# Optimization experiments

Hardware: AMD Instinct MI355X
Metric: run time of the kernel (lower is better)

The kernel has to match this reference:

```python
import jax, jax.numpy as jnp
import numpy as np
import math

B, S, H, N = 64, 512, 768, 16
C_COMP, C_REL = 5, 3
P = N * (N - 1)
LN_EPS = 1e-5

# ordered pair indices (i, j), i != j, row-major like the torch double loop
_PAIR_I, _PAIR_J = np.nonzero(~np.eye(N, dtype=bool))
_PAIR_I = jnp.asarray(_PAIR_I)
_PAIR_J = jnp.asarray(_PAIR_J)


def setup_inputs() -> dict:
    key = jax.random.key(0)
    ks = jax.random.split(key, 20)
    sc = 0.02
    p = lambda k, shape: (jax.random.normal(k, shape, jnp.float32) * sc)
    return {
        "last_hidden_state": jax.random.normal(ks[0], (B, S, H), jnp.float32),
        "span_starts": jax.random.randint(ks[1], (B, N), 0, 480).astype(jnp.int32),
        "span_lengths": jax.random.randint(ks[2], (B, N), 0, 31).astype(jnp.int32),
        "components": jax.random.randint(ks[3], (B, N), 0, C_COMP).astype(jnp.int32),
        "relations": jax.random.randint(ks[4], (B, P), 0, C_REL).astype(jnp.int32),
        # comp_classifier: Linear(H,512) -> Tanh -> Linear(512,C_COMP)
        "comp_w1": p(ks[5], (H, 512)), "comp_b1": jnp.zeros((512,), jnp.float32),
        "comp_w2": p(ks[6], (512, C_COMP)), "comp_b2": jnp.zeros((C_COMP,), jnp.float32),
        # Attention(H, H), no bias
        "wq": p(ks[7], (H, H)), "wk": p(ks[8], (H, H)), "wv": p(ks[9], (H, H)),
        # LayerNorm(H)
        "ln_g": jnp.ones((H,), jnp.float32), "ln_b": jnp.zeros((H,), jnp.float32),
        # rel_classifier: Linear(2H,512) -> Tanh -> Linear(512,C_REL)
        "rel_w1": p(ks[10], (2 * H, 512)), "rel_b1": jnp.zeros((512,), jnp.float32),
        "rel_w2": p(ks[11], (512, C_REL)), "rel_b2": jnp.zeros((C_REL,), jnp.float32),
    }


def _ce_mean(logits, gold):
    # logits [M, C], gold [M] -> scalar mean cross entropy
    logp = jax.nn.log_softmax(logits, axis=-1)
    return -jnp.mean(jnp.take_along_axis(logp, gold[:, None].astype(jnp.int32), axis=-1))


def reference(last_hidden_state, span_starts, span_lengths, components, relations,
              comp_w1, comp_b1, comp_w2, comp_b2,
              wq, wk, wv, ln_g, ln_b,
              rel_w1, rel_b1, rel_w2, rel_b2):
    # --- per-span mean pooling (inclusive end = start + length), masked+vectorized ---
    pos = jnp.arange(S)
    ends = span_starts + span_lengths
    mask = ((pos[None, None, :] >= span_starts[:, :, None]) &
            (pos[None, None, :] <= ends[:, :, None])).astype(jnp.float32)  # [B,N,S]
    lens = (span_lengths + 1).astype(jnp.float32)
    pooled = jnp.einsum('bns,bsh->bnh', mask, last_hidden_state) / lens[:, :, None]  # [B,N,H]
    # dropout(p=0.2) is identity in eval mode

    # --- component classifier ---
    comp_logits = jnp.tanh(pooled @ comp_w1 + comp_b1) @ comp_w2 + comp_b2  # [B,N,C_COMP]

    # --- small self-attention over spans ---
    q = pooled @ wq; k = pooled @ wk; v = pooled @ wv
    scores = jax.nn.softmax(jnp.einsum('bnd,bmd->bnm', q, k) / math.sqrt(H), axis=-1)
    attn = jnp.einsum('bnm,bmh->bnh', scores, v)

    # --- residual + layernorm ---
    x = pooled + attn
    mu = jnp.mean(x, axis=-1, keepdims=True)
    var = jnp.mean((x - mu) ** 2, axis=-1, keepdims=True)
    x = (x - mu) * jax.lax.rsqrt(var + LN_EPS) * ln_g + ln_b  # [B,N,H]

    # --- O(N^2) pairwise relation classification (ordered pairs i != j) ---
    pair_feat = jnp.concatenate([x[:, _PAIR_I, :], x[:, _PAIR_J, :]], axis=-1)  # [B,P,2H]
    rel_logits = jnp.tanh(pair_feat @ rel_w1 + rel_b1) @ rel_w2 + rel_b2  # [B,P,C_REL]

    loss_comp = _ce_mean(comp_logits.reshape(-1, C_COMP), components.reshape(-1))
    loss_rel = _ce_mean(rel_logits.reshape(-1, C_REL), relations.reshape(-1))
    return (comp_logits.reshape(-1, C_COMP), rel_logits.reshape(-1, C_REL), loss_comp, loss_rel)
```

## Files before the change

### kernel.cpp

```cpp
#include <hip/hip_runtime.h>

#define BB 64
#define SS 512
#define HH 768
#define NSPAN 16
#define PP 240
#define CCOMP 5
#define CREL 3

typedef unsigned short u16;
typedef __attribute__((ext_vector_type(8))) short bf16x8;
typedef __attribute__((ext_vector_type(4))) float f32x4;

__device__ __forceinline__ u16 f2bf(float f) {
    union { float f; unsigned int i; } v; v.f = f;
    unsigned int x = v.i;
    unsigned int lsb = (x >> 16) & 1u;
    x += 0x7fffu + lsb;
    return (u16)(x >> 16);
}

__global__ __launch_bounds__(256) void prep_kernel(
    const float* __restrict__ cw1, const float* __restrict__ wq,
    const float* __restrict__ wk, const float* __restrict__ wv,
    const float* __restrict__ rw1, u16* __restrict__ wcat_t, u16* __restrict__ relw_t) {
    int blk = blockIdx.x;
    const float* W; int ldw, nt; u16* outp;
    if (blk < 384)        {             W = cw1; ldw = 512; nt = 16; outp = wcat_t; }
    else if (blk < 960)   { blk -= 384; W = wq;  ldw = 768; nt = 24; outp = wcat_t + (size_t)512 * 768; }
    else if (blk < 1536)  { blk -= 960; W = wk;  ldw = 768; nt = 24; outp = wcat_t + (size_t)1280 * 768; }
    else if (blk < 2112)  { blk -= 1536; W = wv; ldw = 768; nt = 24; outp = wcat_t + (size_t)2048 * 768; }
    else if (blk < 2496)  { blk -= 2112; W = rw1; ldw = 512; nt = 16; outp = relw_t; }
    else                  { blk -= 2496; W = rw1 + (size_t)768 * 512; ldw = 512; nt = 16; outp = relw_t + (size_t)512 * 768; }
    int tk = blk / nt, tn = blk % nt;
    int k0 = tk * 32, n0 = tn * 32;
    __shared__ u16 Ls[32][36];
    int tid = threadIdx.x;
    int tx = tid & 31, ty = tid >> 5;
#pragma unroll
    for (int r = 0; r < 4; ++r) {
        int k = ty + r * 8;
        Ls[tx][k] = f2bf(W[(size_t)(k0 + k) * ldw + n0 + tx]);
    }
    __syncthreads();
#pragma unroll
    for (int r = 0; r < 4; ++r) {
        int n = ty + r * 8;
        outp[(size_t)(n0 + n) * 768 + k0 + tx] = Ls[n][tx];
    }
}

__global__ __launch_bounds__(256) void pool_kernel(
    const float* __restrict__ lhs, const int* __restrict__ starts,
    const int* __restrict__ lens, float* __restrict__ pooled, u16* __restrict__ pooled_bf) {
    int bn = blockIdx.x;
    int b = bn >> 4;
    int st = starts[bn];
    int ln = lens[bn];
    int tid = threadIdx.x;
    const float* base = lhs + ((size_t)b * SS + st) * HH;
    float a0 = 0.f, a1 = 0.f, a2 = 0.f;
    for (int s = 0; s <= ln; ++s) {
        const float* row = base + (size_t)s * HH;
        a0 += row[tid];
        a1 += row[tid + 256];
        a2 += row[tid + 512];
    }
    float inv = 1.0f / (float)(ln + 1);
    a0 *= inv; a1 *= inv; a2 *= inv;
    float* out = pooled + (size_t)bn * HH;
    u16* outb = pooled_bf + (size_t)bn * HH;
    out[tid] = a0;       out[tid + 256] = a1;       out[tid + 512] = a2;
    outb[tid] = f2bf(a0); outb[tid + 256] = f2bf(a1); outb[tid + 512] = f2bf(a2);
}

__device__ __forceinline__ void gemm_mfma_tile(
    const u16* __restrict__ A, const u16* __restrict__ Bt,
    float* __restrict__ C, int ldc, int row0, int ccol0,
    const float* __restrict__ bias, int act) {
    __shared__ u16 As[64][72];
    __shared__ u16 Bs[64][72];
    int tid = threadIdx.x;
    int lane = tid & 63, w = tid >> 6;
    int q = lane >> 4, l15 = lane & 15;
    int wm = (w & 1) * 32, wn = (w >> 1) * 32;
    int r = tid >> 2, c0 = (tid & 3) * 16;
    const u16* ga = A + (size_t)(row0 + r) * 768 + c0;
    const u16* gb = Bt + (size_t)(ccol0 + r) * 768 + c0;
    f32x4 acc[2][2];
#pragma unroll
    for (int i = 0; i < 2; ++i)
#pragma unroll
        for (int j = 0; j < 2; ++j) acc[i][j] = (f32x4){0.f, 0.f, 0.f, 0.f};

    for (int k0 = 0; k0 < 768; k0 += 64) {
        uint4 va0 = *(const uint4*)(ga + k0);
        uint4 va1 = *(const uint4*)(ga + k0 + 8);
        uint4 vb0 = *(const uint4*)(gb + k0);
        uint4 vb1 = *(const uint4*)(gb + k0 + 8);
        __syncthreads();
        *(uint4*)(&As[r][c0]) = va0;
        *(uint4*)(&As[r][c0 + 8]) = va1;
        *(uint4*)(&Bs[r][c0]) = vb0;
        *(uint4*)(&Bs[r][c0 + 8]) = vb1;
        __syncthreads();
#pragma unroll
        for (int ks = 0; ks < 2; ++ks) {
            bf16x8 a0 = *(const bf16x8*)(&As[wm + l15][ks * 32 + q * 8]);
            bf16x8 a1 = *(const bf16x8*)(&As[wm + 16 + l15][ks * 32 + q * 8]);
            bf16x8 b0 = *(const bf16x8*)(&Bs[wn + l15][ks * 32 + q * 8]);
            bf16x8 b1 = *(const bf16x8*)(&Bs[wn + 16 + l15][ks * 32 + q * 8]);
            acc[0][0] = __builtin_amdgcn_mfma_f32_16x16x32_bf16(a0, b0, acc[0][0], 0, 0, 0);
            acc[0][1] = __builtin_amdgcn_mfma_f32_16x16x32_bf16(a0, b1, acc[0][1], 0, 0, 0);
            acc[1][0] = __builtin_amdgcn_mfma_f32_16x16x32_bf16(a1, b0, acc[1][0], 0, 0, 0);
            acc[1][1] = __builtin_amdgcn_mfma_f32_16x16x32_bf16(a1, b1, acc[1][1], 0, 0, 0);
        }
    }
#pragma unroll
    for (int tm = 0; tm < 2; ++tm)
#pragma unroll
        for (int tn = 0; tn < 2; ++tn)
#pragma unroll
            for (int reg = 0; reg < 4; ++reg) {
                int rr = row0 + wm + tm * 16 + q * 4 + reg;
                int cc = ccol0 + wn + tn * 16 + l15;
                float v = acc[tm][tn][reg];
                if (bias) v += bias[cc];
                if (act) v = tanhf(v);
                C[(size_t)rr * ldc + cc] = v;
            }
}

__global__ __launch_bounds__(256) void gemm_pw_kernel(
    const u16* __restrict__ pooled_bf, const u16* __restrict__ wcat_t,
    const float* __restrict__ comp_b1, float* __restrict__ y2) {
    int ccol0 = blockIdx.x * 64;
    int row0 = blockIdx.y * 64;
    int act = (ccol0 < 512);
    gemm_mfma_tile(pooled_bf, wcat_t, y2, 2816, row0, ccol0, act ? comp_b1 : nullptr, act);
}

__global__ __launch_bounds__(256) void gemm_z_kernel(
    const u16* __restrict__ x_bf, const u16* __restrict__ relw_t, float* __restrict__ Z) {
    int ccol0 = blockIdx.x * 64;
    int row0 = blockIdx.y * 64;
    gemm_mfma_tile(x_bf, relw_t, Z, 1024, row0, ccol0, nullptr, 0);
}

__global__ __launch_bounds__(256) void attn_ln_kernel(
    const float* __restrict__ y2, const float* __restrict__ pooled,
    const float* __restrict__ ln_g, const float* __restrict__ ln_b,
    float* __restrict__ x, u16* __restrict__ x_bf) {
    __shared__ float ks[16][772];
    __shared__ float Ssm[16][17];
    int b = blockIdx.x;
    int tid = threadIdx.x;
    int n = tid >> 4;
    int hl = tid & 15;

    for (int u = 0; u < 48; ++u) {
        int h = hl + (u << 4);
        ks[n][h] = y2[((size_t)(b * 16 + n)) * 2816 + 1280 + h];
    }
    __syncthreads();

    int m = tid & 15;
    const float* qrow = y2 + ((size_t)(b * 16 + n)) * 2816 + 512;
    float dot = 0.f;
    for (int h = 0; h < 768; h += 4) {
        float4 qv = *(const float4*)(qrow + h);
        float4 kv = *(const float4*)(&ks[m][h]);
        dot += qv.x * kv.x + qv.y * kv.y + qv.z * kv.z + qv.w * kv.w;
    }
    float sval = dot * 0.03608439182435161f;
    float mx = sval;
#pragma unroll
    for (int off = 8; off >= 1; off >>= 1) mx = fmaxf(mx, __shfl_xor(mx, off, 16));
    float pexp = __expf(sval - mx);
    float psum = pexp;
#pragma unroll
    for (int off = 8; off >= 1; off >>= 1) psum += __shfl_xor(psum, off, 16);
    Ssm[n][m] = pexp / psum;
    __syncthreads();

    for (int u = 0; u < 48; ++u) {
        int h = hl + (u << 4);
        ks[n][h] = y2[((size_t)(b * 16 + n)) * 2816 + 2048 + h];
    }
    __syncthreads();

    float sc[16];
#pragma unroll
    for (int mm = 0; mm < 16; ++mm) sc[mm] = Ssm[n][mm];
    int row = b * 16 + n;
    const float* prow = pooled + (size_t)row * HH;
    float xv[48];
    float ssum = 0.f, ssq = 0.f;
    for (int u = 0; u < 48; ++u) {
        int h = hl + (u << 4);
        float a = 0.f;
#pragma unroll
        for (int mm = 0; mm < 16; ++mm) a += sc[mm] * ks[mm][h];
        float v = prow[h] + a;
        xv[u] = v;
        ssum += v;
        ssq += v * v;
    }
#pragma unroll
    for (int off = 8; off >= 1; off >>= 1) {
        ssum += __shfl_xor(ssum, off, 16);
        ssq += __shfl_xor(ssq, off, 16);
    }
    float mu = ssum * (1.0f / 768.0f);
    float var = ssq * (1.0f / 768.0f) - mu * mu;
    float rs = rsqrtf(var + 1e-5f);
    float* xrow = x + (size_t)row * HH;
    u16* xrow_bf = x_bf + (size_t)row * HH;
    for (int u = 0; u < 48; ++u) {
        int h = hl + (u << 4);
        float v = (xv[u] - mu) * rs * ln_g[h] + ln_b[h];
        xrow[h] = v;
        xrow_bf[h] = f2bf(v);
    }
}

__global__ __launch_bounds__(256) void comp_head_kernel(
    const float* __restrict__ y2, const float* __restrict__ w2,
    const float* __restrict__ b2, const int* __restrict__ gold,
    float* __restrict__ out, float* __restrict__ partial) {
    __shared__ float red[4];
    int wave = threadIdx.x >> 6, lane = threadIdx.x & 63;
    int row = blockIdx.x * 4 + wave;
    const float* hrow = y2 + (size_t)row * 2816;
    float acc[CCOMP] = {0.f, 0.f, 0.f, 0.f, 0.f};
#pragma unroll
    for (int t = 0; t < 8; ++t) {
        int c = lane + (t << 6);
        float h = hrow[c];
#pragma unroll
        for (int cc = 0; cc < CCOMP; ++cc) acc[cc] += h * w2[c * CCOMP + cc];
    }
#pragma unroll
    for (int cc = 0; cc < CCOMP; ++cc)
#pragma unroll
        for (int off = 32; off >= 1; off >>= 1) acc[cc] += __shfl_down(acc[cc], off);
    if (lane == 0) {
        float l[CCOMP];
        float mx = -1e30f;
#pragma unroll
        for (int cc = 0; cc < CCOMP; ++cc) { l[cc] = acc[cc] + b2[cc]; mx = fmaxf(mx, l[cc]); }
        float se = 0.f;
#pragma unroll
        for (int cc = 0; cc < CCOMP; ++cc) se += __expf(l[cc] - mx);
        float lse = __logf(se) + mx;
        red[wave] = lse - l[gold[row]];
#pragma unroll
        for (int cc = 0; cc < CCOMP; ++cc) out[row * CCOMP + cc] = l[cc];
    }
    __syncthreads();
    if (threadIdx.x == 0) partial[blockIdx.x] = red[0] + red[1] + red[2] + red[3];
}

__global__ __launch_bounds__(256) void rel_head_kernel(
    const float* __restrict__ Z, const float* __restrict__ b1,
    const float* __restrict__ w2, const float* __restrict__ b2,
    const int* __restrict__ gold, float* __restrict__ out,
    float* __restrict__ partial) {
    __shared__ float red[4];
    int wave = threadIdx.x >> 6, lane = threadIdx.x & 63;
    int row = blockIdx.x * 4 + wave;
    int b = row / PP;
    int p = row - b * PP;
    int i = p / 15;
    int jj = p - i * 15;
    int j = jj + (jj >= i ? 1 : 0);
    const float* z1 = Z + ((size_t)(b * 16 + i)) * 1024;
    const float* z2 = Z + ((size_t)(b * 16 + j)) * 1024 + 512;
    float a0 = 0.f, a1 = 0.f, a2 = 0.f;
#pragma unroll
    for (int t = 0; t < 8; ++t) {
        int c = lane + (t << 6);
        float h = tanhf(z1[c] + z2[c] + b1[c]);
        a0 += h * w2[c * 3 + 0];
        a1 += h * w2[c * 3 + 1];
        a2 += h * w2[c * 3 + 2];
    }
#pragma unroll
    for (int off = 32; off >= 1; off >>= 1) {
        a0 += __shfl_down(a0, off);
        a1 += __shfl_down(a1, off);
        a2 += __shfl_down(a2, off);
    }
    if (lane == 0) {
        float l0 = a0 + b2[0];
        float l1 = a1 + b2[1];
        float l2 = a2 + b2[2];
        float mx = fmaxf(l0, fmaxf(l1, l2));
        float se = __expf(l0 - mx) + __expf(l1 - mx) + __expf(l2 - mx);
        float lse = __logf(se) + mx;
        int g = gold[row];
        float lg = (g == 0) ? l0 : ((g == 1) ? l1 : l2);
        red[wave] = lse - lg;
        out[row * 3 + 0] = l0;
        out[row * 3 + 1] = l1;
        out[row * 3 + 2] = l2;
    }
    __syncthreads();
    if (threadIdx.x == 0) partial[blockIdx.x] = red[0] + red[1] + red[2] + red[3];
}

__global__ __launch_bounds__(256) void finalize_kernel(
    const float* __restrict__ comp_p, const float* __restrict__ rel_p,
    float* __restrict__ out) {
    __shared__ float rc[4], rr[4];
    int tid = threadIdx.x;
    int wave = tid >> 6, lane = tid & 63;
    float sc = comp_p[tid];
    float sr = 0.f;
#pragma unroll
    for (int k = 0; k < 15; ++k) sr += rel_p[tid + k * 256];
#pragma unroll
    for (int off = 32; off >= 1; off >>= 1) {
        sc += __shfl_down(sc, off);
        sr += __shfl_down(sr, off);
    }
    if (lane == 0) { rc[wave] = sc; rr[wave] = sr; }
    __syncthreads();
    if (tid == 0) {
        out[51200] = (rc[0] + rc[1] + rc[2] + rc[3]) * (1.0f / 1024.0f);
        out[51201] = (rr[0] + rr[1] + rr[2] + rr[3]) * (1.0f / 15360.0f);
    }
}

extern "C" void kernel_launch(void* const* d_in, const int* in_sizes, int n_in,
                              void* d_out, int out_size, void* d_ws, size_t ws_size,
                              hipStream_t stream) {
    const float* lhs     = (const float*)d_in[0];
    const int* starts    = (const int*)d_in[1];
    const int* lens      = (const int*)d_in[2];
    const int* comps     = (const int*)d_in[3];
    const int* rels      = (const int*)d_in[4];
    const float* comp_w1 = (const float*)d_in[5];
    const float* comp_b1 = (const float*)d_in[6];
    const float* comp_w2 = (const float*)d_in[7];
    const float* comp_b2 = (const float*)d_in[8];
    const float* wq      = (const float*)d_in[9];
    const float* wk      = (const float*)d_in[10];
    const float* wv      = (const float*)d_in[11];
    const float* ln_g    = (const float*)d_in[12];
    const float* ln_b    = (const float*)d_in[13];
    const float* rel_w1  = (const float*)d_in[14];
    const float* rel_b1  = (const float*)d_in[15];
    const float* rel_w2  = (const float*)d_in[16];
    const float* rel_b2  = (const float*)d_in[17];
    float* out = (float*)d_out;
    float* ws = (float*)d_ws;

    float* pooled = ws;
    float* y2     = pooled + 786432;
    float* x      = y2 + 2883584;
    float* Z      = x + 786432;
    float* comp_p = Z + 1048576;
    float* rel_p  = comp_p + 256;
    u16* pooled_bf = (u16*)(rel_p + 3840);
    u16* x_bf      = pooled_bf + 786432;
    u16* wcat_t    = x_bf + 786432;
    u16* relw_t    = wcat_t + 2162688;

    prep_kernel<<<2880, 256, 0, stream>>>(comp_w1, wq, wk, wv, rel_w1, wcat_t, relw_t);
    pool_kernel<<<1024, 256, 0, stream>>>(lhs, starts, lens, pooled, pooled_bf);
    gemm_pw_kernel<<<dim3(44, 16), 256, 0, stream>>>(pooled_bf, wcat_t, comp_b1, y2);
    attn_ln_kernel<<<64, 256, 0, stream>>>(y2, pooled, ln_g, ln_b, x, x_bf);
    gemm_z_kernel<<<dim3(16, 16), 256, 0, stream>>>(x_bf, relw_t, Z);
    comp_head_kernel<<<256, 256, 0, stream>>>(y2, comp_w2, comp_b2, comps, out, comp_p);
    rel_head_kernel<<<3840, 256, 0, stream>>>(Z, rel_b1, rel_w2, rel_b2, rels, out + 5120, rel_p);
    finalize_kernel<<<1, 256, 0, stream>>>(comp_p, rel_p, out);
}
```

Measured before the change: 252.2 us.

## Prefetch GEMM tiles, shrink Z tile, fast tanh, merge head kernels, drop fp32 x

Several changes at once. The GEMM kernels now register-prefetch the next K tile while computing the current one. The Z GEMM uses 32-row tiles so more blocks run. tanhf is replaced with an exp-based fast tanh in the GEMM epilogue and the relation head. The comp and rel head kernels are merged into a single launch, and the unused fp32 LayerNorm output write is removed. Together these aim to cut launch overhead, memory latency and transcendental cost, at some risk of slightly different tanh precision.

```diff
diff --git a/kernel.cpp b/kernel.cpp
--- a/kernel.cpp
+++ b/kernel.cpp
@@ -18,6 +18,12 @@
     unsigned int lsb = (x >> 16) & 1u;
     x += 0x7fffu + lsb;
     return (u16)(x >> 16);
+}
+
+__device__ __forceinline__ float ftanh(float x) {
+    float xc = fminf(fmaxf(x, -15.f), 15.f);
+    float e = __expf(2.f * xc);
+    return (e - 1.f) / (e + 1.f);
 }
 
 __global__ __launch_bounds__(256) void prep_kernel(
@@ -74,36 +80,44 @@
     outb[tid] = f2bf(a0); outb[tid + 256] = f2bf(a1); outb[tid + 512] = f2bf(a2);
 }
 
-__device__ __forceinline__ void gemm_mfma_tile(
-    const u16* __restrict__ A, const u16* __restrict__ Bt,
-    float* __restrict__ C, int ldc, int row0, int ccol0,
-    const float* __restrict__ bias, int act) {
+__global__ __launch_bounds__(256) void gemm_pw_kernel(
+    const u16* __restrict__ pooled_bf, const u16* __restrict__ wcat_t,
+    const float* __restrict__ comp_b1, float* __restrict__ y2) {
     __shared__ u16 As[64][72];
     __shared__ u16 Bs[64][72];
+    int ccol0 = blockIdx.x * 64;
+    int row0 = blockIdx.y * 64;
+    int act = (ccol0 < 512);
     int tid = threadIdx.x;
     int lane = tid & 63, w = tid >> 6;
     int q = lane >> 4, l15 = lane & 15;
     int wm = (w & 1) * 32, wn = (w >> 1) * 32;
     int r = tid >> 2, c0 = (tid & 3) * 16;
-    const u16* ga = A + (size_t)(row0 + r) * 768 + c0;
-    const u16* gb = Bt + (size_t)(ccol0 + r) * 768 + c0;
+    const u16* ga = pooled_bf + (size_t)(row0 + r) * 768 + c0;
+    const u16* gb = wcat_t + (size_t)(ccol0 + r) * 768 + c0;
     f32x4 acc[2][2];
 #pragma unroll
     for (int i = 0; i < 2; ++i)
 #pragma unroll
         for (int j = 0; j < 2; ++j) acc[i][j] = (f32x4){0.f, 0.f, 0.f, 0.f};
 
+    uint4 va0 = *(const uint4*)(ga);
+    uint4 va1 = *(const uint4*)(ga + 8);
+    uint4 vb0 = *(const uint4*)(gb);
+    uint4 vb1 = *(const uint4*)(gb + 8);
     for (int k0 = 0; k0 < 768; k0 += 64) {
-        uint4 va0 = *(const uint4*)(ga + k0);
-        uint4 va1 = *(const uint4*)(ga + k0 + 8);
-        uint4 vb0 = *(const uint4*)(gb + k0);
-        uint4 vb1 = *(const uint4*)(gb + k0 + 8);
         __syncthreads();
         *(uint4*)(&As[r][c0]) = va0;
         *(uint4*)(&As[r][c0 + 8]) = va1;
         *(uint4*)(&Bs[r][c0]) = vb0;
         *(uint4*)(&Bs[r][c0 + 8]) = vb1;
         __syncthreads();
+        if (k0 + 64 < 768) {
+            va0 = *(const uint4*)(ga + k0 + 64);
+            va1 = *(const uint4*)(ga + k0 + 72);
+            vb0 = *(const uint4*)(gb + k0 + 64);
+            vb1 = *(const uint4*)(gb + k0 + 72);
+        }
 #pragma unroll
         for (int ks = 0; ks < 2; ++ks) {
             bf16x8 a0 = *(const bf16x8*)(&As[wm + l15][ks * 32 + q * 8]);
@@ -125,32 +139,66 @@
                 int rr = row0 + wm + tm * 16 + q * 4 + reg;
                 int cc = ccol0 + wn + tn * 16 + l15;
                 float v = acc[tm][tn][reg];
-                if (bias) v += bias[cc];
-                if (act) v = tanhf(v);
-                C[(size_t)rr * ldc + cc] = v;
+                if (act) v = ftanh(v + comp_b1[cc]);
+                y2[(size_t)rr * 2816 + cc] = v;
             }
-}
-
-__global__ __launch_bounds__(256) void gemm_pw_kernel(
-    const u16* __restrict__ pooled_bf, const u16* __restrict__ wcat_t,
-    const float* __restrict__ comp_b1, float* __restrict__ y2) {
-    int ccol0 = blockIdx.x * 64;
-    int row0 = blockIdx.y * 64;
-    int act = (ccol0 < 512);
-    gemm_mfma_tile(pooled_bf, wcat_t, y2, 2816, row0, ccol0, act ? comp_b1 : nullptr, act);
 }
 
 __global__ __launch_bounds__(256) void gemm_z_kernel(
     const u16* __restrict__ x_bf, const u16* __restrict__ relw_t, float* __restrict__ Z) {
+    __shared__ u16 As[32][72];
+    __shared__ u16 Bs[64][72];
     int ccol0 = blockIdx.x * 64;
-    int row0 = blockIdx.y * 64;
-    gemm_mfma_tile(x_bf, relw_t, Z, 1024, row0, ccol0, nullptr, 0);
+    int row0 = blockIdx.y * 32;
+    int tid = threadIdx.x;
+    int lane = tid & 63, w = tid >> 6;
+    int q = lane >> 4, l15 = lane & 15;
+    int wm = (w & 1) * 16, wn = (w >> 1) * 32;
+    int ra = tid >> 3, ca = (tid & 7) * 8;
+    int rb = tid >> 2, cb = (tid & 3) * 16;
+    const u16* ga = x_bf + (size_t)(row0 + ra) * 768 + ca;
+    const u16* gb = relw_t + (size_t)(ccol0 + rb) * 768 + cb;
+    f32x4 acc[2];
+    acc[0] = (f32x4){0.f, 0.f, 0.f, 0.f};
+    acc[1] = (f32x4){0.f, 0.f, 0.f, 0.f};
+
+    uint4 va = *(const uint4*)(ga);
+    uint4 vb0 = *(const uint4*)(gb);
+    uint4 vb1 = *(const uint4*)(gb + 8);
+    for (int k0 = 0; k0 < 768; k0 += 64) {
+        __syncthreads();
+        *(uint4*)(&As[ra][ca]) = va;
+        *(uint4*)(&Bs[rb][cb]) = vb0;
+        *(uint4*)(&Bs[rb][cb + 8]) = vb1;
+        __syncthreads();
+        if (k0 + 64 < 768) {
+            va = *(const uint4*)(ga + k0 + 64);
+            vb0 = *(const uint4*)(gb + k0 + 64);
+            vb1 = *(const uint4*)(gb + k0 + 72);
+        }
+#pragma unroll
+        for (int ks = 0; ks < 2; ++ks) {
+            bf16x8 a0 = *(const bf16x8*)(&As[wm + l15][ks * 32 + q * 8]);
+            bf16x8 b0 = *(const bf16x8*)(&Bs[wn + l15][ks * 32 + q * 8]);
+            bf16x8 b1 = *(const bf16x8*)(&Bs[wn + 16 + l15][ks * 32 + q * 8]);
+            acc[0] = __builtin_amdgcn_mfma_f32_16x16x32_bf16(a0, b0, acc[0], 0, 0, 0);
+            acc[1] = __builtin_amdgcn_mfma_f32_16x16x32_bf16(a0, b1, acc[1], 0, 0, 0);
+        }
+    }
+#pragma unroll
+    for (int tn = 0; tn < 2; ++tn)
+#pragma unroll
+        for (int reg = 0; reg < 4; ++reg) {
+            int rr = row0 + wm + q * 4 + reg;
+            int cc = ccol0 + wn + tn * 16 + l15;
+            Z[(size_t)rr * 1024 + cc] = acc[tn][reg];
+        }
 }
 
 __global__ __launch_bounds__(256) void attn_ln_kernel(
     const float* __restrict__ y2, const float* __restrict__ pooled,
     const float* __restrict__ ln_g, const float* __restrict__ ln_b,
-    float* __restrict__ x, u16* __restrict__ x_bf) {
+    u16* __restrict__ x_bf) {
     __shared__ float ks[16][772];
     __shared__ float Ssm[16][17];
     int b = blockIdx.x;
@@ -214,99 +262,92 @@
     float mu = ssum * (1.0f / 768.0f);
     float var = ssq * (1.0f / 768.0f) - mu * mu;
     float rs = rsqrtf(var + 1e-5f);
-    float* xrow = x + (size_t)row * HH;
     u16* xrow_bf = x_bf + (size_t)row * HH;
     for (int u = 0; u < 48; ++u) {
         int h = hl + (u << 4);
-        float v = (xv[u] - mu) * rs * ln_g[h] + ln_b[h];
-        xrow[h] = v;
-        xrow_bf[h] = f2bf(v);
-    }
-}
-
-__global__ __launch_bounds__(256) void comp_head_kernel(
-    const float* __restrict__ y2, const float* __restrict__ w2,
-    const float* __restrict__ b2, const int* __restrict__ gold,
-    float* __restrict__ out, float* __restrict__ partial) {
+        xrow_bf[h] = f2bf((xv[u] - mu) * rs * ln_g[h] + ln_b[h]);
+    }
+}
+
+__global__ __launch_bounds__(256) void heads_kernel(
+    const float* __restrict__ Z, const float* __restrict__ rb1,
+    const float* __restrict__ rw2, const float* __restrict__ rb2,
+    const int* __restrict__ rels,
+    const float* __restrict__ y2, const float* __restrict__ cw2,
+    const float* __restrict__ cb2, const int* __restrict__ comps,
+    float* __restrict__ out, float* __restrict__ rel_p, float* __restrict__ comp_p) {
     __shared__ float red[4];
     int wave = threadIdx.x >> 6, lane = threadIdx.x & 63;
-    int row = blockIdx.x * 4 + wave;
-    const float* hrow = y2 + (size_t)row * 2816;
-    float acc[CCOMP] = {0.f, 0.f, 0.f, 0.f, 0.f};
-#pragma unroll
-    for (int t = 0; t < 8; ++t) {
-        int c = lane + (t << 6);
-        float h = hrow[c];
-#pragma unroll
-        for (int cc = 0; cc < CCOMP; ++cc) acc[cc] += h * w2[c * CCOMP + cc];
-    }
-#pragma unroll
-    for (int cc = 0; cc < CCOMP; ++cc)
-#pragma unroll
-        for (int off = 32; off >= 1; off >>= 1) acc[cc] += __shfl_down(acc[cc], off);
-    if (lane == 0) {
-        float l[CCOMP];
-        float mx = -1e30f;
-#pragma unroll
-        for (int cc = 0; cc < CCOMP; ++cc) { l[cc] = acc[cc] + b2[cc]; mx = fmaxf(mx, l[cc]); }
-        float se = 0.f;
-#pragma unroll
-        for (int cc = 0; cc < CCOMP; ++cc) se += __expf(l[cc] - mx);
-        float lse = __logf(se) + mx;
-        red[wave] = lse - l[gold[row]];
-#pragma unroll
-        for (int cc = 0; cc < CCOMP; ++cc) out[row * CCOMP + cc] = l[cc];
-    }
-    __syncthreads();
-    if (threadIdx.x == 0) partial[blockIdx.x] = red[0] + red[1] + red[2] + red[3];
-}
-
-__global__ __launch_bounds__(256) void rel_head_kernel(
-    const float* __restrict__ Z, const float* __restrict__ b1,
-    const float* __restrict__ w2, const float* __restrict__ b2,
-    const int* __restrict__ gold, float* __restrict__ out,
-    float* __restrict__ partial) {
-    __shared__ float red[4];
-    int wave = threadIdx.x >> 6, lane = threadIdx.x & 63;
-    int row = blockIdx.x * 4 + wave;
-    int b = row / PP;
-    int p = row - b * PP;
-    int i = p / 15;
-    int jj = p - i * 15;
-    int j = jj + (jj >= i ? 1 : 0);
-    const float* z1 = Z + ((size_t)(b * 16 + i)) * 1024;
-    const float* z2 = Z + ((size_t)(b * 16 + j)) * 1024 + 512;
-    float a0 = 0.f, a1 = 0.f, a2 = 0.f;
-#pragma unroll
-    for (int t = 0; t < 8; ++t) {
-        int c = lane + (t << 6);
-        float h = tanhf(z1[c] + z2[c] + b1[c]);
-        a0 += h * w2[c * 3 + 0];
-        a1 += h * w2[c * 3 + 1];
-        a2 += h * w2[c * 3 + 2];
-    }
-#pragma unroll
-    for (int off = 32; off >= 1; off >>= 1) {
-        a0 += __shfl_down(a0, off);
-        a1 += __shfl_down(a1, off);
-        a2 += __shfl_down(a2, off);
-    }
-    if (lane == 0) {
-        float l0 = a0 + b2[0];
-        float l1 = a1 + b2[1];
-        float l2 = a2 + b2[2];
-        float mx = fmaxf(l0, fmaxf(l1, l2));
-        float se = __expf(l0 - mx) + __expf(l1 - mx) + __expf(l2 - mx);
-        float lse = __logf(se) + mx;
-        int g = gold[row];
-        float lg = (g == 0) ? l0 : ((g == 1) ? l1 : l2);
-        red[wave] = lse - lg;
-        out[row * 3 + 0] = l0;
-        out[row * 3 + 1] = l1;
-        out[row * 3 + 2] = l2;
-    }
-    __syncthreads();
-    if (threadIdx.x == 0) partial[blockIdx.x] = red[0] + red[1] + red[2] + red[3];
+    if (blockIdx.x < 3840) {
+        int row = blockIdx.x * 4 + wave;
+        int b = row / PP;
+        int p = row - b * PP;
+        int i = p / 15;
+        int jj = p - i * 15;
+        int j = jj + (jj >= i ? 1 : 0);
+        const float* z1 = Z + ((size_t)(b * 16 + i)) * 1024;
+        const float* z2 = Z + ((size_t)(b * 16 + j)) * 1024 + 512;
+        float a0 = 0.f, a1 = 0.f, a2 = 0.f;
+#pragma unroll
+        for (int t = 0; t < 8; ++t) {
+            int c = lane + (t << 6);
+            float h = ftanh(z1[c] + z2[c] + rb1[c]);
+            a0 += h * rw2[c * 3 + 0];
+            a1 += h * rw2[c * 3 + 1];
+            a2 += h * rw2[c * 3 + 2];
+        }
+#pragma unroll
+        for (int off = 32; off >= 1; off >>= 1) {
+            a0 += __shfl_down(a0, off);
+            a1 += __shfl_down(a1, off);
+            a2 += __shfl_down(a2, off);
+        }
+        if (lane == 0) {
+            float l0 = a0 + rb2[0];
+            float l1 = a1 + rb2[1];
+            float l2 = a2 + rb2[2];
+            float mx = fmaxf(l0, fmaxf(l1, l2));
+            float se = __expf(l0 - mx) + __expf(l1 - mx) + __expf(l2 - mx);
+            float lse = __logf(se) + mx;
+            int g = rels[row];
+            float lg = (g == 0) ? l0 : ((g == 1) ? l1 : l2);
+            red[wave] = lse - lg;
+            float* o = out + 5120 + (size_t)row * 3;
+            o[0] = l0; o[1] = l1; o[2] = l2;
+        }
+        __syncthreads();
+        if (threadIdx.x == 0) rel_p[blockIdx.x] = red[0] + red[1] + red[2] + red[3];
+    } else {
+        int row = (blockIdx.x - 3840) * 4 + wave;
+        const float* hrow = y2 + (size_t)row * 2816;
+        float acc[CCOMP] = {0.f, 0.f, 0.f, 0.f, 0.f};
+#pragma unroll
+        for (int t = 0; t < 8; ++t) {
+            int c = lane + (t << 6);
+            float h = hrow[c];
+#pragma unroll
+            for (int cc = 0; cc < CCOMP; ++cc) acc[cc] += h * cw2[c * CCOMP + cc];
+        }
+#pragma unroll
+        for (int cc = 0; cc < CCOMP; ++cc)
+#pragma unroll
+            for (int off = 32; off >= 1; off >>= 1) acc[cc] += __shfl_down(acc[cc], off);
+        if (lane == 0) {
+            float l[CCOMP];
+            float mx = -1e30f;
+#pragma unroll
+            for (int cc = 0; cc < CCOMP; ++cc) { l[cc] = acc[cc] + cb2[cc]; mx = fmaxf(mx, l[cc]); }
+            float se = 0.f;
+#pragma unroll
+            for (int cc = 0; cc < CCOMP; ++cc) se += __expf(l[cc] - mx);
+            float lse = __logf(se) + mx;
+            red[wave] = lse - l[comps[row]];
+#pragma unroll
+            for (int cc = 0; cc < CCOMP; ++cc) out[row * CCOMP + cc] = l[cc];
+        }
+        __syncthreads();
+        if (threadIdx.x == 0) comp_p[blockIdx.x - 3840] = red[0] + red[1] + red[2] + red[3];
+    }
 }
 
 __global__ __launch_bounds__(256) void finalize_kernel(
@@ -358,8 +399,7 @@
 
     float* pooled = ws;
     float* y2     = pooled + 786432;
-    float* x      = y2 + 2883584;
-    float* Z      = x + 786432;
+    float* Z      = y2 + 2883584;
     float* comp_p = Z + 1048576;
     float* rel_p  = comp_p + 256;
     u16* pooled_bf = (u16*)(rel_p + 3840);
@@ -370,9 +410,10 @@
     prep_kernel<<<2880, 256, 0, stream>>>(comp_w1, wq, wk, wv, rel_w1, wcat_t, relw_t);
     pool_kernel<<<1024, 256, 0, stream>>>(lhs, starts, lens, pooled, pooled_bf);
     gemm_pw_kernel<<<dim3(44, 16), 256, 0, stream>>>(pooled_bf, wcat_t, comp_b1, y2);
-    attn_ln_kernel<<<64, 256, 0, stream>>>(y2, pooled, ln_g, ln_b, x, x_bf);
-    gemm_z_kernel<<<dim3(16, 16), 256, 0, stream>>>(x_bf, relw_t, Z);
-    comp_head_kernel<<<256, 256, 0, stream>>>(y2, comp_w2, comp_b2, comps, out, comp_p);
-    rel_head_kernel<<<3840, 256, 0, stream>>>(Z, rel_b1, rel_w2, rel_b2, rels, out + 5120, rel_p);
+    attn_ln_kernel<<<64, 256, 0, stream>>>(y2, pooled, ln_g, ln_b, x_bf);
+    gemm_z_kernel<<<dim3(16, 32), 256, 0, stream>>>(x_bf, relw_t, Z);
+    heads_kernel<<<4096, 256, 0, stream>>>(Z, rel_b1, rel_w2, rel_b2, rels,
+                                           y2, comp_w2, comp_b2, comps,
+                                           out, rel_p, comp_p);
     finalize_kernel<<<1, 256, 0, stream>>>(comp_p, rel_p, out);
 }
```

Result: faster. 243.2 us (-3.6%).
